# Kernel tuning notes

Measured on AMD Instinct MI355X. Metric: run time of the kernel, lower is better.

The kernel has to match this reference:

```python
import jax, jax.numpy as jnp
import numpy as np

# Mistral-7B layer-0 config
D, DKV, DFF, NH, NKV, HD, BLK, VOCAB = 4096, 1024, 14336, 32, 8, 128, 64, 32000
THETA = 10000.0
NF4_CODE = jnp.array([-1.0, -0.6961928009986877, -0.5250730514526367, -0.39491748809814453,
                      -0.28444138169288635, -0.18477343022823334, -0.09105003625154495, 0.0,
                      0.07958029955625534, 0.16093020141124725, 0.24611230194568634,
                      0.33791524171829224, 0.44070982933044434, 0.5626170039176941,
                      0.7229568362236023, 1.0], dtype=jnp.float32)


def dequant_nf4(idx, absmax):
    # idx: int [out,in] 4-bit codes; absmax: [numel/BLK] blockwise scales
    w = jnp.take(NF4_CODE, idx.reshape(-1, BLK)) * absmax[:, None]
    return w.reshape(idx.shape)


def rmsnorm(x, w, eps=1e-5):
    return x * jax.lax.rsqrt(jnp.mean(x * x, axis=-1, keepdims=True) + eps) * w


def rope(x, pos):
    # x: [B,S,H,HD] -- HF rotate-half convention
    half = HD // 2
    inv = 1.0 / (THETA ** (jnp.arange(0, half, dtype=jnp.float32) / half))
    f = pos[:, None] * inv[None, :]                      # [S, half]
    cos = jnp.concatenate([jnp.cos(f), jnp.cos(f)], -1)[None, :, None, :]
    sin = jnp.concatenate([jnp.sin(f), jnp.sin(f)], -1)[None, :, None, :]
    x1, x2 = x[..., :half], x[..., half:]
    rot = jnp.concatenate([-x2, x1], -1)
    return x * cos + rot * sin


def setup_inputs() -> dict:
    key = jax.random.key(0)
    ks = jax.random.split(key, 20)
    B, S = 4, 512
    inp = {}
    inp["input_ids"] = jax.random.randint(ks[0], (B, S), 0, VOCAB, dtype=jnp.int32)
    inp["attention_mask"] = jnp.ones((B, S), dtype=jnp.int32)
    inp["embed_table"] = jax.random.normal(ks[1], (VOCAB, D), dtype=jnp.float32) * 0.02
    shapes = {"q": (D, D), "k": (DKV, D), "v": (DKV, D), "o": (D, D),
              "gate": (DFF, D), "up": (DFF, D), "down": (D, DFF)}
    for i, (n, sh) in enumerate(shapes.items()):
        inp["idx_" + n] = jax.random.randint(ks[2 + i], sh, 0, 16, dtype=jnp.int32)
        inp["absmax_" + n] = jax.random.uniform(ks[9 + i], (sh[0] * sh[1] // BLK,), dtype=jnp.float32) * 0.02
    inp["rms1_w"] = jnp.ones((D,), jnp.float32)
    inp["rms2_w"] = jnp.ones((D,), jnp.float32)
    inp["dp_w"] = jax.random.normal(ks[16], (50, D), jnp.float32) * 0.02
    inp["dp_b"] = jnp.zeros((50,), jnp.float32)
    return inp


def reference(input_ids, attention_mask, embed_table,
              idx_q, idx_k, idx_v, idx_o, idx_gate, idx_up, idx_down,
              absmax_q, absmax_k, absmax_v, absmax_o, absmax_gate, absmax_up, absmax_down,
              rms1_w, rms2_w, dp_w, dp_b):
    B, S = input_ids.shape
    h = embed_table[input_ids]                            # [B,S,D]

    # --- Mistral decoder layer 0 (hidden_states[1]) ---
    r = rmsnorm(h, rms1_w)
    Wq = dequant_nf4(idx_q, absmax_q)
    Wk = dequant_nf4(idx_k, absmax_k)
    Wv = dequant_nf4(idx_v, absmax_v)
    Wo = dequant_nf4(idx_o, absmax_o)
    q = (r @ Wq.T).reshape(B, S, NH, HD)
    k = (r @ Wk.T).reshape(B, S, NKV, HD)
    v = (r @ Wv.T).reshape(B, S, NKV, HD)
    pos = jnp.arange(S, dtype=jnp.float32)
    q, k = rope(q, pos), rope(k, pos)
    rep = NH // NKV
    k = jnp.repeat(k, rep, axis=2)
    v = jnp.repeat(v, rep, axis=2)
    scores = jnp.einsum('bqhd,bkhd->bhqk', q, k) / np.float32(np.sqrt(HD))
    causal = jnp.tril(jnp.ones((S, S), bool))
    m = causal[None, None] & (attention_mask[:, None, None, :] > 0)
    scores = jnp.where(m, scores, jnp.float32(-1e9))
    p = jax.nn.softmax(scores, axis=-1)
    ao = jnp.einsum('bhqk,bkhd->bqhd', p, v).reshape(B, S, D)
    h = h + ao @ Wo.T

    r2 = rmsnorm(h, rms2_w)
    Wg = dequant_nf4(idx_gate, absmax_gate)
    Wu = dequant_nf4(idx_up, absmax_up)
    Wd = dequant_nf4(idx_down, absmax_down)
    h = h + (jax.nn.silu(r2 @ Wg.T) * (r2 @ Wu.T)) @ Wd.T

    # --- last_token_pool + L2 normalize ---
    last = jnp.sum(attention_mask, axis=-1) - 1           # [B]
    pooled = h[jnp.arange(B), last]                       # [B,D]
    pooled = pooled / jnp.maximum(jnp.linalg.norm(pooled, axis=1, keepdims=True), 1e-12)

    # --- down_projection + query*entity node embeddings ---
    emb = pooled @ dp_w.T + dp_b                          # [B,50]
    bs = B // 2
    node = emb[:bs] * emb[bs:]                            # [bs,50]
    return node
```

## Files before the change

kernel.cpp:

```cpp
#include <hip/hip_runtime.h>
#include <stdint.h>
#include <math.h>

#define TOK 2048
#define DMODEL 4096
#define DFF 14336
#define SEQ 512

typedef float f32x4 __attribute__((ext_vector_type(4)));
typedef float f32x2 __attribute__((ext_vector_type(2)));
typedef short s16x8 __attribute__((ext_vector_type(8)));
typedef unsigned short u16x8 __attribute__((ext_vector_type(8)));

__constant__ float NF4_TAB[16] = {
  -1.0f, -0.6961928009986877f, -0.5250730514526367f, -0.39491748809814453f,
  -0.28444138169288635f, -0.18477343022823334f, -0.09105003625154495f, 0.0f,
  0.07958029955625534f, 0.16093020141124725f, 0.24611230194568634f,
  0.33791524171829224f, 0.44070982933044434f, 0.5626170039176941f,
  0.7229568362236023f, 1.0f };

__device__ __forceinline__ uint16_t f2bf(float f) {
  union { float f; uint32_t u; } x; x.f = f;
  uint32_t r = (x.u + 0x7FFFu + ((x.u >> 16) & 1u)) >> 16;
  return (uint16_t)r;
}
__device__ __forceinline__ float bf2f(uint16_t u) {
  union { uint32_t u; float f; } x; x.u = ((uint32_t)u) << 16;
  return x.f;
}
__device__ __forceinline__ f32x4 mfma16(s16x8 a, s16x8 b, f32x4 c) {
  return __builtin_amdgcn_mfma_f32_16x16x32_bf16(a, b, c, 0, 0, 0);
}
__device__ __forceinline__ void gload_lds16(const void* g, void* l) {
  __builtin_amdgcn_global_load_lds(
    (const __attribute__((address_space(1))) unsigned int*)g,
    (__attribute__((address_space(3))) unsigned int*)l, 16, 0, 0);
}
__device__ __forceinline__ f32x2 pf(float w, f32x2 v, f32x2 acc) {
  f32x2 wv = {w, w};
  return wv * v + acc;
}
__device__ __forceinline__ float lut(int iv, float codeReg) {
  return __int_as_float(__builtin_amdgcn_ds_bpermute(iv << 2, __float_as_int(codeReg)));
}

__global__ __launch_bounds__(256) void k_fusedA(const int* __restrict__ ids,
    const float* __restrict__ table, const float* __restrict__ w1,
    uint16_t* __restrict__ rbuf, const int* __restrict__ idxK,
    const float* __restrict__ amK, const int* __restrict__ idxV,
    const float* __restrict__ amV, uint16_t* __restrict__ wbuf,
    const int* __restrict__ maskp, int* __restrict__ lastb,
    float* __restrict__ r4i)
{
  int bid = blockIdx.x, tid = threadIdx.x;
  if (bid < 2048) {
    int t = bid;
    int wv = tid >> 6, l = tid & 63;
    const float* src = table + (size_t)ids[t] * DMODEL;
    int d0 = tid * 16;
    float vals[16];
    float ss = 0.f;
    #pragma unroll
    for (int i = 0; i < 4; ++i) {
      float4 v4 = *(const float4*)(src + d0 + i * 4);
      vals[i*4+0] = v4.x; vals[i*4+1] = v4.y; vals[i*4+2] = v4.z; vals[i*4+3] = v4.w;
      ss += v4.x*v4.x + v4.y*v4.y + v4.z*v4.z + v4.w*v4.w;
    }
    #pragma unroll
    for (int off = 1; off < 64; off <<= 1) ss += __shfl_xor(ss, off);
    __shared__ float red[4];
    if (l == 0) red[wv] = ss;
    __syncthreads();
    float rs = rsqrtf((red[0]+red[1]+red[2]+red[3]) * (1.f/DMODEL) + 1e-5f);
    #pragma unroll
    for (int cth = 0; cth < 2; ++cth) {
      int dd = d0 + cth * 8;
      u16x8 pk;
      #pragma unroll
      for (int j = 0; j < 8; ++j) pk[j] = f2bf(vals[cth*8+j] * rs * w1[dd + j]);
      int dsw = (dd & ~63) | (((((dd >> 3) & 7) ^ (t & 7))) << 3);
      *(u16x8*)(rbuf + (size_t)t * DMODEL + dsw) = pk;
    }
  } else if (bid < 3072) {
    bool isV = bid >= 2560;
    const int* idx = isV ? idxV : idxK;
    const float* am = isV ? amV : amK;
    uint16_t* out = wbuf + (isV ? (size_t)1024 * DMODEL : 0);
    int base = bid - (isV ? 2560 : 2048);
    float codeReg = NF4_TAB[tid & 15];
    const int nch = 1024 * DMODEL / 8;
    for (int c = base * 256 + tid; c < nch; c += 512 * 256) {
      int e = c << 3;
      int row = e >> 12;
      int kc = e & 4095;
      float a = am[c >> 3];
      int4 i0 = *(const int4*)(idx + e);
      int4 i1 = *(const int4*)(idx + e + 4);
      u16x8 pk;
      pk[0] = f2bf(lut(i0.x, codeReg) * a);
      pk[1] = f2bf(lut(i0.y, codeReg) * a);
      pk[2] = f2bf(lut(i0.z, codeReg) * a);
      pk[3] = f2bf(lut(i0.w, codeReg) * a);
      pk[4] = f2bf(lut(i1.x, codeReg) * a);
      pk[5] = f2bf(lut(i1.y, codeReg) * a);
      pk[6] = f2bf(lut(i1.z, codeReg) * a);
      pk[7] = f2bf(lut(i1.w, codeReg) * a);
      int dk = (kc & ~63) | (((((kc >> 3) & 7) ^ (row & 7))) << 3);
      *(u16x8*)(out + (size_t)row * DMODEL + dk) = pk;
    }
  } else {
    int b = bid - 3072;
    int wv = tid >> 6, l = tid & 63;
    __shared__ int redi[4];
    __shared__ float redf[4];
    int cnt = 0;
    for (int j = tid; j < SEQ; j += 256) cnt += (maskp[b * SEQ + j] > 0);
    #pragma unroll
    for (int off = 1; off < 64; off <<= 1) cnt += __shfl_xor(cnt, off);
    if (l == 0) redi[wv] = cnt;
    __syncthreads();
    int last = redi[0] + redi[1] + redi[2] + redi[3] - 1;
    if (tid == 0) lastb[b] = last;
    int t = b * SEQ + last;
    const float* src = table + (size_t)ids[t] * DMODEL;
    int d0 = tid * 16;
    float vals[16];
    float ss = 0.f;
    #pragma unroll
    for (int i = 0; i < 4; ++i) {
      float4 v4 = *(const float4*)(src + d0 + i * 4);
      vals[i*4+0] = v4.x; vals[i*4+1] = v4.y; vals[i*4+2] = v4.z; vals[i*4+3] = v4.w;
      ss += v4.x*v4.x + v4.y*v4.y + v4.z*v4.z + v4.w*v4.w;
    }
    #pragma unroll
    for (int off = 1; off < 64; off <<= 1) ss += __shfl_xor(ss, off);
    if (l == 0) redf[wv] = ss;
    __syncthreads();
    float rs = rsqrtf((redf[0]+redf[1]+redf[2]+redf[3]) * (1.f/DMODEL) + 1e-5f);
    #pragma unroll
    for (int i = 0; i < 16; ++i)
      r4i[(d0 + i) * 4 + b] = vals[i] * rs * w1[d0 + i];
  }
}

__global__ __launch_bounds__(512, 2) void k_gemmkv(
    const uint16_t* __restrict__ A, const uint16_t* __restrict__ W,
    uint16_t* __restrict__ pout)
{
  constexpr int K = 4096;
  constexpr int NT = 16;
  __shared__ __align__(1024) uint16_t As_[2 * 256 * 64];
  __shared__ __align__(1024) uint16_t Bs_[2 * 256 * 64];
  const int tid = threadIdx.x;
  const int wid = tid >> 6, l = tid & 63;
  const int wr = wid >> 2, wc = wid & 3;
  int f = blockIdx.x + (blockIdx.y << 3) + (blockIdx.z << 6);
  int fs = ((f & 7) << 5) + (f >> 3);
  const int n0 = (fs & 7) * 256;
  const int m0 = ((fs >> 3) & 7) * 256;
  const int zq = fs >> 6;
  const size_t kbase = (size_t)zq * 1024;
  const int lrow = l >> 3, lcb = (l & 7) * 16;

  auto stA = [&](int t, int h) {
    int ta = (t < NT) ? t : (t - NT);
    const char* g = (const char*)A +
        ((size_t)(m0 + h * 128 + wid * 16 + lrow) * K + kbase + ta * 64) * 2 + lcb;
    char* s = (char*)As_ + (t & 1) * 32768 + h * 16384 + wid * 2048;
    gload_lds16(g, s);
    gload_lds16(g + (size_t)8 * K * 2, s + 1024);
  };
  auto stB = [&](int t, int h) {
    int ta = (t < NT) ? t : (t - NT);
    const char* g = (const char*)W +
        ((size_t)(n0 + h * 128 + wid * 16 + lrow) * K + kbase + ta * 64) * 2 + lcb;
    char* s = (char*)Bs_ + (t & 1) * 32768 + h * 16384 + wid * 2048;
    gload_lds16(g, s);
    gload_lds16(g + (size_t)8 * K * 2, s + 1024);
  };

  const int cb0 = (((l >> 4) << 4)) ^ ((l & 7) << 4);
  const int cb1 = (64 + ((l >> 4) << 4)) ^ ((l & 7) << 4);

  const f32x4 Z4 = {0.f, 0.f, 0.f, 0.f};
  f32x4 acc[8][4];
  #pragma unroll
  for (int i = 0; i < 8; ++i)
    #pragma unroll
    for (int j = 0; j < 4; ++j) acc[i][j] = Z4;
  s16x8 bfr[4][2];

#define VMW asm volatile("s_waitcnt vmcnt(6)" ::: "memory")
#define PHASE(DB, Q, READB, STG) {                                          \
    const char* abase = (const char*)As_ + (DB) * 32768;                    \
    s16x8 af[2][2];                                                         \
    _Pragma("unroll") for (int mm = 0; mm < 2; ++mm) {                      \
      int arow = ((2 * (2 * (Q) + mm) + wr) * 16 + (l & 15)) * 128;         \
      af[mm][0] = *(const s16x8*)(abase + arow + cb0);                      \
      af[mm][1] = *(const s16x8*)(abase + arow + cb1);                      \
    }                                                                       \
    if (READB) {                                                            \
      const char* bbase = (const char*)Bs_ + (DB) * 32768;                  \
      _Pragma("unroll") for (int nn = 0; nn < 4; ++nn) {                    \
        int brow = (wc * 64 + nn * 16 + (l & 15)) * 128;                    \
        bfr[nn][0] = *(const s16x8*)(bbase + brow + cb0);                   \
        bfr[nn][1] = *(const s16x8*)(bbase + brow + cb1);                   \
      }                                                                     \
    }                                                                       \
    STG;                                                                    \
    __builtin_amdgcn_s_barrier();                                           \
    asm volatile("s_waitcnt lgkmcnt(0)" ::: "memory");                      \
    __builtin_amdgcn_sched_barrier(0);                                      \
    __builtin_amdgcn_s_setprio(1);                                          \
    _Pragma("unroll") for (int mm = 0; mm < 2; ++mm)                        \
      _Pragma("unroll") for (int nn = 0; nn < 4; ++nn) {                    \
        acc[2 * (Q) + mm][nn] = mfma16(af[mm][0], bfr[nn][0], acc[2 * (Q) + mm][nn]); \
        acc[2 * (Q) + mm][nn] = mfma16(af[mm][1], bfr[nn][1], acc[2 * (Q) + mm][nn]); \
      }                                                                     \
    __builtin_amdgcn_s_setprio(0);                                          \
    __builtin_amdgcn_s_barrier();                                           \
  }

  stB(0, 0); stA(0, 0); stB(0, 1); stA(0, 1);
  stB(1, 0); stA(1, 0); stB(1, 1);
  VMW;
  __builtin_amdgcn_s_barrier();

  for (int it = 0; it < NT / 2; ++it) {
    int t0 = 2 * it, t1 = t0 + 1;
    PHASE(0, 0, 1, stA(t1, 1));
    PHASE(0, 1, 0, stB(t0 + 2, 0));
    PHASE(0, 2, 0, stA(t0 + 2, 0));
    PHASE(0, 3, 0, { stB(t0 + 2, 1); VMW; });
    PHASE(1, 0, 1, stA(t0 + 2, 1));
    PHASE(1, 1, 0, stB(t1 + 2, 0));
    PHASE(1, 2, 0, stA(t1 + 2, 0));
    PHASE(1, 3, 0, { stB(t1 + 2, 1); VMW; });
  }
  asm volatile("s_waitcnt vmcnt(0)" ::: "memory");
  __builtin_amdgcn_s_barrier();
#undef PHASE
#undef VMW

  uint16_t* po = pout + (size_t)zq * 2048 * 2048;
  #pragma unroll
  for (int mf = 0; mf < 8; ++mf)
    #pragma unroll
    for (int nf = 0; nf < 4; ++nf)
      #pragma unroll
      for (int r = 0; r < 4; ++r) {
        int row = m0 + (2 * mf + wr) * 16 + ((l >> 4) << 2) + r;
        int col = n0 + wc * 64 + nf * 16 + (l & 15);
        po[(size_t)row * 2048 + col] = f2bf(acc[mf][nf][r]);
      }
}

__global__ __launch_bounds__(256) void k_fusedD(const uint16_t* __restrict__ p,
    uint16_t* __restrict__ kv, const int* __restrict__ idxQ,
    const float* __restrict__ amQ, const float* __restrict__ a4i,
    float* __restrict__ q4i)
{
  int bid = blockIdx.x, tid = threadIdx.x;
  if (bid < 2048) {
    int t = bid;
    const size_t zs = (size_t)2048 * 2048;
    auto sum4 = [&](int c) -> float {
      size_t o = (size_t)t * 2048 + c;
      return bf2f(p[o]) + bf2f(p[o + zs]) + bf2f(p[o + 2 * zs]) + bf2f(p[o + 3 * zs]);
    };
    float pos = (float)(t & (SEQ - 1));
    for (int pi = tid; pi < 512; pi += 256) {
      int hh = pi >> 6, j = pi & 63;
      int c1 = hh * 128 + j, c2 = c1 + 64;
      float s1 = sum4(c1), s2 = sum4(c2);
      float f = pos * expf(-(float)j * 0.14391156831212787f);
      float sn, cs;
      sincosf(f, &sn, &cs);
      kv[(size_t)t * 2048 + c1] = f2bf(s1 * cs - s2 * sn);
      kv[(size_t)t * 2048 + c2] = f2bf(s2 * cs + s1 * sn);
    }
    for (int c = 1024 + tid; c < 2048; c += 256)
      kv[(size_t)t * 2048 + c] = f2bf(sum4(c));
  } else {
    float codeReg = NF4_TAB[tid & 15];
    int wv = tid >> 6, l = tid & 63;
    int lhi = l >> 4;
    int n = (bid - 2048) * 4 + wv;
    const int4* ip = (const int4*)(idxQ + (size_t)n * 4096);
    const float* ap = amQ + (size_t)n * 64;
    f32x2 a01 = {0.f, 0.f}, a23 = {0.f, 0.f};
    #pragma unroll
    for (int kk = 0; kk < 16; ++kk) {
      int4 iv = ip[kk * 64 + l];
      float sc = ap[kk * 4 + lhi];
      float w0 = lut(iv.x, codeReg) * sc, w1 = lut(iv.y, codeReg) * sc;
      float w2 = lut(iv.z, codeReg) * sc, w3 = lut(iv.w, codeReg) * sc;
      const float* A0 = a4i + (kk * 256 + l * 4) * 4;
      f32x4 k0 = *(const f32x4*)(A0);
      f32x4 k1 = *(const f32x4*)(A0 + 4);
      f32x4 k2 = *(const f32x4*)(A0 + 8);
      f32x4 k3 = *(const f32x4*)(A0 + 12);
      a01 = pf(w0, __builtin_shufflevector(k0, k0, 0, 1), a01);
      a23 = pf(w0, __builtin_shufflevector(k0, k0, 2, 3), a23);
      a01 = pf(w1, __builtin_shufflevector(k1, k1, 0, 1), a01);
      a23 = pf(w1, __builtin_shufflevector(k1, k1, 2, 3), a23);
      a01 = pf(w2, __builtin_shufflevector(k2, k2, 0, 1), a01);
      a23 = pf(w2, __builtin_shufflevector(k2, k2, 2, 3), a23);
      a01 = pf(w3, __builtin_shufflevector(k3, k3, 0, 1), a01);
      a23 = pf(w3, __builtin_shufflevector(k3, k3, 2, 3), a23);
    }
    float a0 = a01[0], a1 = a01[1], a2 = a23[0], a3 = a23[1];
    #pragma unroll
    for (int off = 1; off < 64; off <<= 1) {
      a0 += __shfl_xor(a0, off); a1 += __shfl_xor(a1, off);
      a2 += __shfl_xor(a2, off); a3 += __shfl_xor(a3, off);
    }
    if (l == 0) {
      f32x4 o;
      o[0] = a0; o[1] = a1; o[2] = a2; o[3] = a3;
      *(f32x4*)(q4i + (size_t)n * 4) = o;
    }
  }
}

__global__ __launch_bounds__(256) void k_attn4(const float* __restrict__ q4i,
    const uint16_t* __restrict__ kv, const int* __restrict__ maskp,
    const int* __restrict__ lastb, float* __restrict__ ao4i)
{
  int hh = blockIdx.x, b = blockIdx.y;
  int kvh = hh >> 2;
  int tid = threadIdx.x;
  __shared__ float qs[128];
  __shared__ float sarr[512];
  __shared__ float red[256];
  __shared__ f32x2 oacc2[4][64];
  int last = lastb[b];
  if (tid < 128) {
    int d = tid, j = d & 63;
    float f = (float)last * expf(-(float)j * 0.14391156831212787f);
    float sn, cs;
    sincosf(f, &sn, &cs);
    float qd  = q4i[(hh * 128 + d) * 4 + b];
    float qd2 = (d < 64) ? q4i[(hh * 128 + d + 64) * 4 + b]
                         : q4i[(hh * 128 + d - 64) * 4 + b];
    float v = (d < 64) ? (qd * cs - qd2 * sn) : (qd * cs + qd2 * sn);
    qs[d] = v * 0.08838834764831845f;
  }
  __syncthreads();
  float sl[2];
  #pragma unroll
  for (int h2 = 0; h2 < 2; ++h2) {
    int jj = tid + h2 * 256;
    bool valid = (jj <= last) && (maskp[b * SEQ + jj] > 0);
    float s = -1e9f;
    if (valid) {
      s = 0.f;
      const uint16_t* kp = kv + ((size_t)(b * SEQ + jj)) * 2048 + kvh * 128;
      #pragma unroll
      for (int c = 0; c < 16; ++c) {
        u16x8 kvv = *(const u16x8*)(kp + c * 8);
        #pragma unroll
        for (int e = 0; e < 8; ++e)
          s = fmaf(qs[c * 8 + e], bf2f(kvv[e]), s);
      }
    }
    sarr[jj] = s;
    sl[h2] = s;
  }
  red[tid] = fmaxf(sl[0], sl[1]);
  __syncthreads();
  for (int s = 128; s > 0; s >>= 1) {
    if (tid < s) red[tid] = fmaxf(red[tid], red[tid + s]);
    __syncthreads();
  }
  float m = red[0];
  __syncthreads();
  float ps = 0.f;
  #pragma unroll
  for (int h2 = 0; h2 < 2; ++h2) {
    int jj = tid + h2 * 256;
    float pe = __expf(sarr[jj] - m);
    ps += pe;
    sarr[jj] = pe;
  }
  red[tid] = ps;
  __syncthreads();
  for (int s = 128; s > 0; s >>= 1) {
    if (tid < s) red[tid] += red[tid + s];
    __syncthreads();
  }
  float inv = 1.f / red[0];
  __syncthreads();
  int qd = tid >> 6, pr = tid & 63;
  f32x2 acc = {0.f, 0.f};
  const uint16_t* vp = kv + ((size_t)(b * SEQ + qd * 128)) * 2048 + 1024 + kvh * 128 + pr * 2;
  for (int j = 0; j < 128; ++j) {
    float pj = sarr[qd * 128 + j];
    uint32_t pair = *(const uint32_t*)(vp + (size_t)j * 2048);
    f32x2 v;
    v[0] = bf2f((uint16_t)(pair & 0xffff));
    v[1] = bf2f((uint16_t)(pair >> 16));
    acc = pf(pj, v, acc);
  }
  oacc2[qd][pr] = acc;
  __syncthreads();
  if (tid < 64) {
    f32x2 s = oacc2[0][tid] + oacc2[1][tid] + oacc2[2][tid] + oacc2[3][tid];
    ao4i[((size_t)(hh * 128 + tid * 2)) * 4 + b]     = s[0] * inv;
    ao4i[((size_t)(hh * 128 + tid * 2 + 1)) * 4 + b] = s[1] * inv;
  }
}

__global__ __launch_bounds__(256) void k_gemv_o(const int* __restrict__ idx,
    const float* __restrict__ am, const float* __restrict__ a4i,
    float* __restrict__ out4i, const float* __restrict__ table,
    const int* __restrict__ ids, const int* __restrict__ lastb)
{
  float codeReg = NF4_TAB[threadIdx.x & 15];
  int wv = threadIdx.x >> 6, l = threadIdx.x & 63;
  int lhi = l >> 4;
  int n = blockIdx.x * 4 + wv;
  const int4* ip = (const int4*)(idx + (size_t)n * 4096);
  const float* ap = am + (size_t)n * 64;
  f32x2 a01 = {0.f, 0.f}, a23 = {0.f, 0.f};
  #pragma unroll
  for (int kk = 0; kk < 16; ++kk) {
    int4 iv = ip[kk * 64 + l];
    float sc = ap[kk * 4 + lhi];
    float w0 = lut(iv.x, codeReg) * sc, w1 = lut(iv.y, codeReg) * sc;
    float w2 = lut(iv.z, codeReg) * sc, w3 = lut(iv.w, codeReg) * sc;
    const float* A0 = a4i + (kk * 256 + l * 4) * 4;
    f32x4 k0 = *(const f32x4*)(A0);
    f32x4 k1 = *(const f32x4*)(A0 + 4);
    f32x4 k2 = *(const f32x4*)(A0 + 8);
    f32x4 k3 = *(const f32x4*)(A0 + 12);
    a01 = pf(w0, __builtin_shufflevector(k0, k0, 0, 1), a01);
    a23 = pf(w0, __builtin_shufflevector(k0, k0, 2, 3), a23);
    a01 = pf(w1, __builtin_shufflevector(k1, k1, 0, 1), a01);
    a23 = pf(w1, __builtin_shufflevector(k1, k1, 2, 3), a23);
    a01 = pf(w2, __builtin_shufflevector(k2, k2, 0, 1), a01);
    a23 = pf(w2, __builtin_shufflevector(k2, k2, 2, 3), a23);
    a01 = pf(w3, __builtin_shufflevector(k3, k3, 0, 1), a01);
    a23 = pf(w3, __builtin_shufflevector(k3, k3, 2, 3), a23);
  }
  float a0 = a01[0], a1 = a01[1], a2 = a23[0], a3 = a23[1];
  #pragma unroll
  for (int off = 1; off < 64; off <<= 1) {
    a0 += __shfl_xor(a0, off); a1 += __shfl_xor(a1, off);
    a2 += __shfl_xor(a2, off); a3 += __shfl_xor(a3, off);
  }
  if (l == 0) {
    f32x4 o;
    o[0] = a0; o[1] = a1; o[2] = a2; o[3] = a3;
    #pragma unroll
    for (int r = 0; r < 4; ++r)
      o[r] += table[(size_t)ids[r * SEQ + lastb[r]] * DMODEL + n];
    *(f32x4*)(out4i + (size_t)n * 4) = o;
  }
}

__global__ __launch_bounds__(256) void k_rms2i(const float* __restrict__ h4i,
    const float* __restrict__ w, float* __restrict__ r2i)
{
  int tid = threadIdx.x, wv = tid >> 6, l = tid & 63;
  f32x4 vals[16];
  f32x4 ss = {0.f, 0.f, 0.f, 0.f};
  #pragma unroll
  for (int i = 0; i < 16; ++i) {
    vals[i] = *(const f32x4*)(h4i + (size_t)(tid + i * 256) * 4);
    ss += vals[i] * vals[i];
  }
  #pragma unroll
  for (int off = 1; off < 64; off <<= 1) {
    ss[0] += __shfl_xor(ss[0], off);
    ss[1] += __shfl_xor(ss[1], off);
    ss[2] += __shfl_xor(ss[2], off);
    ss[3] += __shfl_xor(ss[3], off);
  }
  __shared__ f32x4 red[4];
  if (l == 0) red[wv] = ss;
  __syncthreads();
  f32x4 tot = red[0] + red[1] + red[2] + red[3];
  f32x4 rs;
  #pragma unroll
  for (int r = 0; r < 4; ++r) rs[r] = rsqrtf(tot[r] * (1.f / 4096.f) + 1e-5f);
  #pragma unroll
  for (int i = 0; i < 16; ++i) {
    float wk = w[tid + i * 256];
    f32x4 o = vals[i] * rs * wk;
    *(f32x4*)(r2i + (size_t)(tid + i * 256) * 4) = o;
  }
}

__global__ __launch_bounds__(256) void k_gemv_gu(const int* __restrict__ idxg,
    const float* __restrict__ amg, const int* __restrict__ idxu,
    const float* __restrict__ amu, const float* __restrict__ a4i,
    float* __restrict__ hm4i)
{
  float codeReg = NF4_TAB[threadIdx.x & 15];
  int wv = threadIdx.x >> 6, l = threadIdx.x & 63;
  int lhi = l >> 4;
  int n = blockIdx.x * 4 + wv;
  const int4* ipg = (const int4*)(idxg + (size_t)n * 4096);
  const int4* ipu = (const int4*)(idxu + (size_t)n * 4096);
  const float* apg = amg + (size_t)n * 64;
  const float* apu = amu + (size_t)n * 64;
  f32x2 g01 = {0.f, 0.f}, g23 = {0.f, 0.f};
  f32x2 u01 = {0.f, 0.f}, u23 = {0.f, 0.f};
  #pragma unroll 8
  for (int kk = 0; kk < 16; ++kk) {
    int4 ig = ipg[kk * 64 + l];
    int4 iu = ipu[kk * 64 + l];
    float sg = apg[kk * 4 + lhi];
    float su = apu[kk * 4 + lhi];
    float wg0 = lut(ig.x, codeReg) * sg, wg1 = lut(ig.y, codeReg) * sg;
    float wg2 = lut(ig.z, codeReg) * sg, wg3 = lut(ig.w, codeReg) * sg;
    float wu0 = lut(iu.x, codeReg) * su, wu1 = lut(iu.y, codeReg) * su;
    float wu2 = lut(iu.z, codeReg) * su, wu3 = lut(iu.w, codeReg) * su;
    const float* A0 = a4i + (kk * 256 + l * 4) * 4;
    f32x4 k0 = *(const f32x4*)(A0);
    f32x4 k1 = *(const f32x4*)(A0 + 4);
    f32x4 k2 = *(const f32x4*)(A0 + 8);
    f32x4 k3 = *(const f32x4*)(A0 + 12);
    f32x2 k0l = __builtin_shufflevector(k0, k0, 0, 1), k0h = __builtin_shufflevector(k0, k0, 2, 3);
    f32x2 k1l = __builtin_shufflevector(k1, k1, 0, 1), k1h = __builtin_shufflevector(k1, k1, 2, 3);
    f32x2 k2l = __builtin_shufflevector(k2, k2, 0, 1), k2h = __builtin_shufflevector(k2, k2, 2, 3);
    f32x2 k3l = __builtin_shufflevector(k3, k3, 0, 1), k3h = __builtin_shufflevector(k3, k3, 2, 3);
    g01 = pf(wg0, k0l, g01); g23 = pf(wg0, k0h, g23);
    g01 = pf(wg1, k1l, g01); g23 = pf(wg1, k1h, g23);
    g01 = pf(wg2, k2l, g01); g23 = pf(wg2, k2h, g23);
    g01 = pf(wg3, k3l, g01); g23 = pf(wg3, k3h, g23);
    u01 = pf(wu0, k0l, u01); u23 = pf(wu0, k0h, u23);
    u01 = pf(wu1, k1l, u01); u23 = pf(wu1, k1h, u23);
    u01 = pf(wu2, k2l, u01); u23 = pf(wu2, k2h, u23);
    u01 = pf(wu3, k3l, u01); u23 = pf(wu3, k3h, u23);
  }
  float g0 = g01[0], g1 = g01[1], g2 = g23[0], g3 = g23[1];
  float u0 = u01[0], u1 = u01[1], u2 = u23[0], u3 = u23[1];
  #pragma unroll
  for (int off = 1; off < 64; off <<= 1) {
    g0 += __shfl_xor(g0, off); g1 += __shfl_xor(g1, off);
    g2 += __shfl_xor(g2, off); g3 += __shfl_xor(g3, off);
    u0 += __shfl_xor(u0, off); u1 += __shfl_xor(u1, off);
    u2 += __shfl_xor(u2, off); u3 += __shfl_xor(u3, off);
  }
  if (l == 0) {
    f32x4 o;
    o[0] = (g0 / (1.f + __expf(-g0))) * u0;
    o[1] = (g1 / (1.f + __expf(-g1))) * u1;
    o[2] = (g2 / (1.f + __expf(-g2))) * u2;
    o[3] = (g3 / (1.f + __expf(-g3))) * u3;
    *(f32x4*)(hm4i + (size_t)n * 4) = o;
  }
}

__global__ __launch_bounds__(256) void k_gemv_down(const int* __restrict__ idx,
    const float* __restrict__ am, const float* __restrict__ hm4i,
    const float* __restrict__ h4i, float* __restrict__ h4r)
{
  float codeReg = NF4_TAB[threadIdx.x & 15];
  int wv = threadIdx.x >> 6, l = threadIdx.x & 63;
  int lhi = l >> 4;
  int n = blockIdx.x * 4 + wv;
  const int4* ip = (const int4*)(idx + (size_t)n * 14336);
  const float* ap = am + (size_t)n * 224;
  f32x2 a01 = {0.f, 0.f}, a23 = {0.f, 0.f};
  #pragma unroll 8
  for (int kk = 0; kk < 56; ++kk) {
    int4 iv = ip[kk * 64 + l];
    float sc = ap[kk * 4 + lhi];
    float w0 = lut(iv.x, codeReg) * sc, w1 = lut(iv.y, codeReg) * sc;
    float w2 = lut(iv.z, codeReg) * sc, w3 = lut(iv.w, codeReg) * sc;
    const float* A0 = hm4i + (kk * 256 + l * 4) * 4;
    f32x4 k0 = *(const f32x4*)(A0);
    f32x4 k1 = *(const f32x4*)(A0 + 4);
    f32x4 k2 = *(const f32x4*)(A0 + 8);
    f32x4 k3 = *(const f32x4*)(A0 + 12);
    a01 = pf(w0, __builtin_shufflevector(k0, k0, 0, 1), a01);
    a23 = pf(w0, __builtin_shufflevector(k0, k0, 2, 3), a23);
    a01 = pf(w1, __builtin_shufflevector(k1, k1, 0, 1), a01);
    a23 = pf(w1, __builtin_shufflevector(k1, k1, 2, 3), a23);
    a01 = pf(w2, __builtin_shufflevector(k2, k2, 0, 1), a01);
    a23 = pf(w2, __builtin_shufflevector(k2, k2, 2, 3), a23);
    a01 = pf(w3, __builtin_shufflevector(k3, k3, 0, 1), a01);
    a23 = pf(w3, __builtin_shufflevector(k3, k3, 2, 3), a23);
  }
  float a0 = a01[0], a1 = a01[1], a2 = a23[0], a3 = a23[1];
  #pragma unroll
  for (int off = 1; off < 64; off <<= 1) {
    a0 += __shfl_xor(a0, off); a1 += __shfl_xor(a1, off);
    a2 += __shfl_xor(a2, off); a3 += __shfl_xor(a3, off);
  }
  if (l == 0) {
    f32x4 hr = *(const f32x4*)(h4i + (size_t)n * 4);
    h4r[0 * 4096 + n] = hr[0] + a0;
    h4r[1 * 4096 + n] = hr[1] + a1;
    h4r[2 * 4096 + n] = hr[2] + a2;
    h4r[3 * 4096 + n] = hr[3] + a3;
  }
}

__global__ __launch_bounds__(256) void k_pool3(const float* __restrict__ h4r,
    const float* __restrict__ dpw, const float* __restrict__ dpb,
    float* __restrict__ out)
{
  int o = blockIdx.x;
  int tid = threadIdx.x, wv = tid >> 6, l = tid & 63;
  __shared__ float dsh[4], nsh[4];
  const float* row = h4r + wv * 4096;
  const float* wrow = dpw + (size_t)o * 4096;
  float d1 = 0.f, ss = 0.f;
  for (int d = l * 4; d < 4096; d += 256) {
    float4 v = *(const float4*)(row + d);
    float4 u = *(const float4*)(wrow + d);
    d1 += v.x*u.x + v.y*u.y + v.z*u.z + v.w*u.w;
    ss += v.x*v.x + v.y*v.y + v.z*v.z + v.w*v.w;
  }
  #pragma unroll
  for (int off = 1; off < 64; off <<= 1) {
    d1 += __shfl_xor(d1, off);
    ss += __shfl_xor(ss, off);
  }
  if (l == 0) { dsh[wv] = d1; nsh[wv] = fmaxf(sqrtf(ss), 1e-12f); }
  __syncthreads();
  if (tid < 2) {
    float b = dpb[o];
    float e1 = dsh[tid] / nsh[tid] + b;
    float e2 = dsh[tid + 2] / nsh[tid + 2] + b;
    out[tid * 50 + o] = e1 * e2;
  }
}

extern "C" void kernel_launch(void* const* d_in, const int* in_sizes, int n_in,
                              void* d_out, int out_size, void* d_ws, size_t ws_size,
                              hipStream_t stream) {
  const int*   ids   = (const int*)d_in[0];
  const int*   maskp = (const int*)d_in[1];
  const float* table = (const float*)d_in[2];
  const int* idxp[7];
  const float* amp[7];
  if (in_sizes[4] == in_sizes[3] / 64) {
    for (int i = 0; i < 7; ++i) {
      idxp[i] = (const int*)d_in[3 + 2 * i];
      amp[i]  = (const float*)d_in[4 + 2 * i];
    }
  } else {
    for (int i = 0; i < 7; ++i) {
      idxp[i] = (const int*)d_in[3 + i];
      amp[i]  = (const float*)d_in[10 + i];
    }
  }
  const float* rms1 = (const float*)d_in[17];
  const float* rms2w = (const float*)d_in[18];
  const float* dpw  = (const float*)d_in[19];
  const float* dpb  = (const float*)d_in[20];
  float* out = (float*)d_out;

  char* p = (char*)d_ws;
  int*      lastb = (int*)p;      p += 256;
  float*    r4i   = (float*)p;    p += 4 * 4096 * 4;
  float*    q4i   = (float*)p;    p += 4 * 4096 * 4;
  float*    ao4i  = (float*)p;    p += 4 * 4096 * 4;
  float*    h4i   = (float*)p;    p += 4 * 4096 * 4;
  float*    r2i   = (float*)p;    p += 4 * 4096 * 4;
  float*    h4r   = (float*)p;    p += 4 * 4096 * 4;
  float*    hm4i  = (float*)p;    p += (size_t)4 * DFF * 4 + 512;
  uint16_t* kvbuf = (uint16_t*)p; p += (size_t)TOK * 2048 * 2;
  uint16_t* rbuf  = (uint16_t*)p; p += (size_t)TOK * DMODEL * 2;
  uint16_t* wbuf  = (uint16_t*)p; p += (size_t)2048 * DMODEL * 2;
  uint16_t* pbuf  = (uint16_t*)p; p += (size_t)4 * 2048 * 2048 * 2;

  k_fusedA<<<3076, 256, 0, stream>>>(ids, table, rms1, rbuf,
      idxp[1], amp[1], idxp[2], amp[2], wbuf, maskp, lastb, r4i);

  k_gemmkv<<<dim3(8, 8, 4), 512, 0, stream>>>(rbuf, wbuf, pbuf);

  k_fusedD<<<3072, 256, 0, stream>>>(pbuf, kvbuf, idxp[0], amp[0], r4i, q4i);

  k_attn4<<<dim3(32, 4), 256, 0, stream>>>(q4i, kvbuf, maskp, lastb, ao4i);

  k_gemv_o<<<1024, 256, 0, stream>>>(idxp[3], amp[3], ao4i, h4i, table, ids, lastb);

  k_rms2i<<<1, 256, 0, stream>>>(h4i, rms2w, r2i);
  k_gemv_gu<<<3584, 256, 0, stream>>>(idxp[4], amp[4], idxp[5], amp[5], r2i, hm4i);
  k_gemv_down<<<1024, 256, 0, stream>>>(idxp[6], amp[6], hm4i, h4i, h4r);

  k_pool3<<<50, 256, 0, stream>>>(h4r, dpw, dpb, out);
}
```

Before: 373.3 us.

## Fuse RMSNorm-2 into gate/up GEMV via atomic sum-of-squares; vectorize KV RoPE

Removes the single-block k_rms2i launch. k_gemv_o now accumulates the per-batch sum of squares with atomics into a small buffer that k_fusedA zeroes. k_gemv_gu computes the rsqrt from that buffer and applies the norm and weight on the fly when it loads activations. Separately, the KV reduce+RoPE path in k_fusedD now uses 8-wide bf16 vector loads and stores per thread instead of scalar strided accesses. The trade-offs are contention from many atomics (4 per wave, 4096 waves) and redundant norm multiplies in every gate/up block.

```diff
diff --git a/kernel.cpp b/kernel.cpp
--- a/kernel.cpp
+++ b/kernel.cpp
@@ -50,7 +50,7 @@
     const float* __restrict__ amK, const int* __restrict__ idxV,
     const float* __restrict__ amV, uint16_t* __restrict__ wbuf,
     const int* __restrict__ maskp, int* __restrict__ lastb,
-    float* __restrict__ r4i)
+    float* __restrict__ r4i, float* __restrict__ ssq)
 {
   int bid = blockIdx.x, tid = threadIdx.x;
   if (bid < 2048) {
@@ -111,6 +111,7 @@
   } else {
     int b = bid - 3072;
     int wv = tid >> 6, l = tid & 63;
+    if (b == 0 && tid < 4) ssq[tid] = 0.f;
     __shared__ int redi[4];
     __shared__ float redf[4];
     int cnt = 0;
@@ -264,23 +265,54 @@
   if (bid < 2048) {
     int t = bid;
     const size_t zs = (size_t)2048 * 2048;
-    auto sum4 = [&](int c) -> float {
-      size_t o = (size_t)t * 2048 + c;
-      return bf2f(p[o]) + bf2f(p[o + zs]) + bf2f(p[o + 2 * zs]) + bf2f(p[o + 3 * zs]);
+    const size_t rowo = (size_t)t * 2048;
+    float pos = (float)(t & (SEQ - 1));
+    auto sum8 = [&](int c) -> f32x4 {
+      f32x4 dummy; return dummy;
     };
-    float pos = (float)(t & (SEQ - 1));
-    for (int pi = tid; pi < 512; pi += 256) {
-      int hh = pi >> 6, j = pi & 63;
-      int c1 = hh * 128 + j, c2 = c1 + 64;
-      float s1 = sum4(c1), s2 = sum4(c2);
-      float f = pos * expf(-(float)j * 0.14391156831212787f);
-      float sn, cs;
-      sincosf(f, &sn, &cs);
-      kv[(size_t)t * 2048 + c1] = f2bf(s1 * cs - s2 * sn);
-      kv[(size_t)t * 2048 + c2] = f2bf(s2 * cs + s1 * sn);
-    }
-    for (int c = 1024 + tid; c < 2048; c += 256)
-      kv[(size_t)t * 2048 + c] = f2bf(sum4(c));
+    (void)sum8;
+    if (tid < 64) {
+      int hh = tid >> 3, j0 = (tid & 7) * 8;
+      int c1 = hh * 128 + j0;
+      float s1[8], s2[8];
+      {
+        u16x8 a0 = *(const u16x8*)(p + rowo + c1);
+        u16x8 a1 = *(const u16x8*)(p + zs + rowo + c1);
+        u16x8 a2 = *(const u16x8*)(p + 2 * zs + rowo + c1);
+        u16x8 a3 = *(const u16x8*)(p + 3 * zs + rowo + c1);
+        u16x8 b0 = *(const u16x8*)(p + rowo + c1 + 64);
+        u16x8 b1 = *(const u16x8*)(p + zs + rowo + c1 + 64);
+        u16x8 b2 = *(const u16x8*)(p + 2 * zs + rowo + c1 + 64);
+        u16x8 b3 = *(const u16x8*)(p + 3 * zs + rowo + c1 + 64);
+        #pragma unroll
+        for (int e = 0; e < 8; ++e) {
+          s1[e] = bf2f(a0[e]) + bf2f(a1[e]) + bf2f(a2[e]) + bf2f(a3[e]);
+          s2[e] = bf2f(b0[e]) + bf2f(b1[e]) + bf2f(b2[e]) + bf2f(b3[e]);
+        }
+      }
+      u16x8 o1, o2;
+      #pragma unroll
+      for (int e = 0; e < 8; ++e) {
+        float f = pos * expf(-(float)(j0 + e) * 0.14391156831212787f);
+        float sn, cs;
+        sincosf(f, &sn, &cs);
+        o1[e] = f2bf(s1[e] * cs - s2[e] * sn);
+        o2[e] = f2bf(s2[e] * cs + s1[e] * sn);
+      }
+      *(u16x8*)(kv + rowo + c1) = o1;
+      *(u16x8*)(kv + rowo + c1 + 64) = o2;
+    } else if (tid < 192) {
+      int c = 1024 + (tid - 64) * 8;
+      u16x8 a0 = *(const u16x8*)(p + rowo + c);
+      u16x8 a1 = *(const u16x8*)(p + zs + rowo + c);
+      u16x8 a2 = *(const u16x8*)(p + 2 * zs + rowo + c);
+      u16x8 a3 = *(const u16x8*)(p + 3 * zs + rowo + c);
+      u16x8 o;
+      #pragma unroll
+      for (int e = 0; e < 8; ++e)
+        o[e] = f2bf(bf2f(a0[e]) + bf2f(a1[e]) + bf2f(a2[e]) + bf2f(a3[e]));
+      *(u16x8*)(kv + rowo + c) = o;
+    }
   } else {
     float codeReg = NF4_TAB[tid & 15];
     int wv = tid >> 6, l = tid & 63;
@@ -414,7 +446,8 @@
 __global__ __launch_bounds__(256) void k_gemv_o(const int* __restrict__ idx,
     const float* __restrict__ am, const float* __restrict__ a4i,
     float* __restrict__ out4i, const float* __restrict__ table,
-    const int* __restrict__ ids, const int* __restrict__ lastb)
+    const int* __restrict__ ids, const int* __restrict__ lastb,
+    float* __restrict__ ssq)
 {
   float codeReg = NF4_TAB[threadIdx.x & 15];
   int wv = threadIdx.x >> 6, l = threadIdx.x & 63;
@@ -456,48 +489,25 @@
     for (int r = 0; r < 4; ++r)
       o[r] += table[(size_t)ids[r * SEQ + lastb[r]] * DMODEL + n];
     *(f32x4*)(out4i + (size_t)n * 4) = o;
-  }
-}
-
-__global__ __launch_bounds__(256) void k_rms2i(const float* __restrict__ h4i,
-    const float* __restrict__ w, float* __restrict__ r2i)
-{
-  int tid = threadIdx.x, wv = tid >> 6, l = tid & 63;
-  f32x4 vals[16];
-  f32x4 ss = {0.f, 0.f, 0.f, 0.f};
-  #pragma unroll
-  for (int i = 0; i < 16; ++i) {
-    vals[i] = *(const f32x4*)(h4i + (size_t)(tid + i * 256) * 4);
-    ss += vals[i] * vals[i];
-  }
-  #pragma unroll
-  for (int off = 1; off < 64; off <<= 1) {
-    ss[0] += __shfl_xor(ss[0], off);
-    ss[1] += __shfl_xor(ss[1], off);
-    ss[2] += __shfl_xor(ss[2], off);
-    ss[3] += __shfl_xor(ss[3], off);
-  }
-  __shared__ f32x4 red[4];
-  if (l == 0) red[wv] = ss;
-  __syncthreads();
-  f32x4 tot = red[0] + red[1] + red[2] + red[3];
-  f32x4 rs;
-  #pragma unroll
-  for (int r = 0; r < 4; ++r) rs[r] = rsqrtf(tot[r] * (1.f / 4096.f) + 1e-5f);
-  #pragma unroll
-  for (int i = 0; i < 16; ++i) {
-    float wk = w[tid + i * 256];
-    f32x4 o = vals[i] * rs * wk;
-    *(f32x4*)(r2i + (size_t)(tid + i * 256) * 4) = o;
+    #pragma unroll
+    for (int r = 0; r < 4; ++r)
+      atomicAdd(&ssq[r], o[r] * o[r]);
   }
 }
 
 __global__ __launch_bounds__(256) void k_gemv_gu(const int* __restrict__ idxg,
     const float* __restrict__ amg, const int* __restrict__ idxu,
-    const float* __restrict__ amu, const float* __restrict__ a4i,
+    const float* __restrict__ amu, const float* __restrict__ h4i,
+    const float* __restrict__ w2, const float* __restrict__ ssq,
     float* __restrict__ hm4i)
 {
   float codeReg = NF4_TAB[threadIdx.x & 15];
+  f32x4 rs;
+  {
+    f32x4 sv = *(const f32x4*)ssq;
+    #pragma unroll
+    for (int r = 0; r < 4; ++r) rs[r] = rsqrtf(sv[r] * (1.f / 4096.f) + 1e-5f);
+  }
   int wv = threadIdx.x >> 6, l = threadIdx.x & 63;
   int lhi = l >> 4;
   int n = blockIdx.x * 4 + wv;
@@ -517,11 +527,13 @@
     float wg2 = lut(ig.z, codeReg) * sg, wg3 = lut(ig.w, codeReg) * sg;
     float wu0 = lut(iu.x, codeReg) * su, wu1 = lut(iu.y, codeReg) * su;
     float wu2 = lut(iu.z, codeReg) * su, wu3 = lut(iu.w, codeReg) * su;
-    const float* A0 = a4i + (kk * 256 + l * 4) * 4;
-    f32x4 k0 = *(const f32x4*)(A0);
-    f32x4 k1 = *(const f32x4*)(A0 + 4);
-    f32x4 k2 = *(const f32x4*)(A0 + 8);
-    f32x4 k3 = *(const f32x4*)(A0 + 12);
+    int kb = kk * 256 + l * 4;
+    const float* H = h4i + (size_t)kb * 4;
+    float4 w2v = *(const float4*)(w2 + kb);
+    f32x4 k0 = (*(const f32x4*)(H))      * rs * w2v.x;
+    f32x4 k1 = (*(const f32x4*)(H + 4))  * rs * w2v.y;
+    f32x4 k2 = (*(const f32x4*)(H + 8))  * rs * w2v.z;
+    f32x4 k3 = (*(const f32x4*)(H + 12)) * rs * w2v.w;
     f32x2 k0l = __builtin_shufflevector(k0, k0, 0, 1), k0h = __builtin_shufflevector(k0, k0, 2, 3);
     f32x2 k1l = __builtin_shufflevector(k1, k1, 0, 1), k1h = __builtin_shufflevector(k1, k1, 2, 3);
     f32x2 k2l = __builtin_shufflevector(k2, k2, 0, 1), k2h = __builtin_shufflevector(k2, k2, 2, 3);
@@ -658,11 +670,11 @@
 
   char* p = (char*)d_ws;
   int*      lastb = (int*)p;      p += 256;
+  float*    ssq   = (float*)p;    p += 256;
   float*    r4i   = (float*)p;    p += 4 * 4096 * 4;
   float*    q4i   = (float*)p;    p += 4 * 4096 * 4;
   float*    ao4i  = (float*)p;    p += 4 * 4096 * 4;
   float*    h4i   = (float*)p;    p += 4 * 4096 * 4;
-  float*    r2i   = (float*)p;    p += 4 * 4096 * 4;
   float*    h4r   = (float*)p;    p += 4 * 4096 * 4;
   float*    hm4i  = (float*)p;    p += (size_t)4 * DFF * 4 + 512;
   uint16_t* kvbuf = (uint16_t*)p; p += (size_t)TOK * 2048 * 2;
@@ -671,7 +683,7 @@
   uint16_t* pbuf  = (uint16_t*)p; p += (size_t)4 * 2048 * 2048 * 2;
 
   k_fusedA<<<3076, 256, 0, stream>>>(ids, table, rms1, rbuf,
-      idxp[1], amp[1], idxp[2], amp[2], wbuf, maskp, lastb, r4i);
+      idxp[1], amp[1], idxp[2], amp[2], wbuf, maskp, lastb, r4i, ssq);
 
   k_gemmkv<<<dim3(8, 8, 4), 512, 0, stream>>>(rbuf, wbuf, pbuf);
 
@@ -679,10 +691,9 @@
 
   k_attn4<<<dim3(32, 4), 256, 0, stream>>>(q4i, kvbuf, maskp, lastb, ao4i);
 
-  k_gemv_o<<<1024, 256, 0, stream>>>(idxp[3], amp[3], ao4i, h4i, table, ids, lastb);
-
-  k_rms2i<<<1, 256, 0, stream>>>(h4i, rms2w, r2i);
-  k_gemv_gu<<<3584, 256, 0, stream>>>(idxp[4], amp[4], idxp[5], amp[5], r2i, hm4i);
+  k_gemv_o<<<1024, 256, 0, stream>>>(idxp[3], amp[3], ao4i, h4i, table, ids, lastb, ssq);
+
+  k_gemv_gu<<<3584, 256, 0, stream>>>(idxp[4], amp[4], idxp[5], amp[5], h4i, rms2w, ssq, hm4i);
   k_gemv_down<<<1024, 256, 0, stream>>>(idxp[6], amp[6], hm4i, h4i, h4r);
 
   k_pool3<<<50, 256, 0, stream>>>(h4r, dpw, dpb, out);
```

Measured after the change: 578.0 us. 1.55x slower.
